# Performance work log

Hardware: AMD Instinct MI355X
Metric: run time of the kernel (lower is better)

Reference implementation:

```python
import jax, jax.numpy as jnp
import numpy as np

N, E, C, RB, H = 10000, 160000, 64, 8, 64
AVG_NEIGH = 16.0


def _sph(v):
    # component-normalized real spherical harmonics l=1,2,3 of unit vectors v [E,3]
    x, y, z = v[..., 0], v[..., 1], v[..., 2]
    s3, s5, s15 = 3.0 ** 0.5, 5.0 ** 0.5, 15.0 ** 0.5
    y1 = s3 * jnp.stack([x, y, z], -1)  # [E,3]
    y2 = jnp.stack([
        s15 * x * y,
        s15 * y * z,
        0.5 * s5 * (3.0 * z * z - 1.0),
        s15 * x * z,
        0.5 * s15 * (x * x - y * y),
    ], -1)  # [E,5]
    c1 = (35.0 / 8.0) ** 0.5
    c2 = 105.0 ** 0.5
    c3 = (21.0 / 8.0) ** 0.5
    c4 = (7.0 ** 0.5) / 2.0
    y3 = jnp.stack([
        c1 * y * (3.0 * x * x - y * y),
        c2 * x * y * z,
        c3 * y * (5.0 * z * z - 1.0),
        c4 * z * (5.0 * z * z - 3.0),
        c3 * x * (5.0 * z * z - 1.0),
        0.5 * c2 * z * (x * x - y * y),
        c1 * x * (x * x - y * y),
    ], -1)  # [E,7]
    return y1, y2, y3


def setup_inputs() -> dict:
    key = jax.random.key(0)
    ks = jax.random.split(key, 12)
    inp = {
        'vectors': jax.random.normal(ks[0], (E, 3), jnp.float32),
        'node_feats': jax.random.normal(ks[1], (N, C), jnp.float32),
        'radial_embedding': jax.random.normal(ks[2], (E, RB), jnp.float32),
        'W_up': jax.random.normal(ks[3], (C, C), jnp.float32) / np.sqrt(C),
        'mlp_w1': jax.random.normal(ks[4], (RB, H), jnp.float32) / np.sqrt(RB),
        'mlp_w2': jax.random.normal(ks[5], (H, H), jnp.float32) / np.sqrt(H),
        'mlp_w3': jax.random.normal(ks[6], (H, H), jnp.float32) / np.sqrt(H),
        'mlp_w4': jax.random.normal(ks[7], (H, 4 * C), jnp.float32) / np.sqrt(H),
        'W_down': jax.random.normal(ks[8], (4, C, C), jnp.float32) / np.sqrt(C),
        'senders': jax.random.randint(ks[9], (E,), 0, N, jnp.int32),
        'receivers': jax.random.randint(ks[10], (E,), 0, N, jnp.int32),
    }
    return inp


def reference(vectors, node_feats, radial_embedding, W_up, mlp_w1, mlp_w2, mlp_w3, mlp_w4, W_down, senders, receivers):
    n = node_feats.shape[0]
    # linear_up (scalars: plain channel mixing)
    x = node_feats @ W_up                                   # [N,C]
    sf = x[senders]                                         # [E,C] gather
    u = vectors / (jnp.linalg.norm(vectors, axis=-1, keepdims=True) + 1e-12)
    y1, y2, y3 = _sph(u)
    # radial MLP -> per-irrep mixing weights [E, 4C]
    h = jax.nn.silu(radial_embedding @ mlp_w1)
    h = jax.nn.silu(h @ mlp_w2)
    h = jax.nn.silu(h @ mlp_w3)
    mix = h @ mlp_w4
    m0, m1, m2, m3 = jnp.split(mix, 4, axis=-1)             # each [E,C]
    # tensor product of Cx0e with Y_l -> Cx(l), scaled by radial mix
    msg0 = sf * m0                                          # [E,C]
    msg1 = (sf * m1)[:, :, None] * y1[:, None, :]           # [E,C,3]
    msg2 = (sf * m2)[:, :, None] * y2[:, None, :]           # [E,C,5]
    msg3 = (sf * m3)[:, :, None] * y3[:, None, :]           # [E,C,7]
    inv = 1.0 / jnp.sqrt(jnp.asarray(AVG_NEIGH, msg0.dtype))
    seg = lambda m: jax.ops.segment_sum(m, receivers, num_segments=n) * inv
    o0, o1, o2, o3 = seg(msg0), seg(msg1), seg(msg2), seg(msg3)
    # linear_down: per-l channel mixing
    o0 = o0 @ W_down[0]
    o1 = jnp.einsum('ncm,cd->ndm', o1, W_down[1])
    o2 = jnp.einsum('ncm,cd->ndm', o2, W_down[2])
    o3 = jnp.einsum('ncm,cd->ndm', o3, W_down[3])
    return jnp.concatenate([o0, o1.reshape(n, -1), o2.reshape(n, -1), o3.reshape(n, -1)], axis=-1)  # [N, 16C]
```

## Files before the change

### kernel.cpp

```cpp
#include <hip/hip_runtime.h>
#include <math.h>

#define CC 64
typedef _Float16 f16;
typedef _Float16 half8_t __attribute__((ext_vector_type(8)));
typedef float f32x4 __attribute__((ext_vector_type(4)));

__device__ __forceinline__ float silu_f(float v) {
    return v / (1.0f + __expf(-v));
}

__global__ __launch_bounds__(256) void k_pre(
        const float* __restrict__ nf, const float* __restrict__ Wup,
        float* __restrict__ x, int N,
        const float* __restrict__ w1, const float* __restrict__ w2,
        const float* __restrict__ w3, const float* __restrict__ w4,
        const float* __restrict__ Wd,
        f16* __restrict__ wT1, f16* __restrict__ wT2,
        f16* __restrict__ wT3, f16* __restrict__ wT4,
        float* __restrict__ wpack,
        const int* __restrict__ rcv, int* __restrict__ cnt, int E) {
    int nb_up = (N * CC + 255) >> 8;
    int b = blockIdx.x;
    if (b < nb_up) {
        int tid = b * 256 + threadIdx.x;
        if (tid >= N * CC) return;
        int n = tid >> 6;
        int j = tid & 63;
        const float* nfr = nf + (size_t)n * CC;
        float acc = 0.f;
#pragma unroll
        for (int k = 0; k < CC; ++k) acc += nfr[k] * Wup[k * CC + j];
        x[tid] = acc;
    } else if (b < nb_up + 168) {
        int i = (b - nb_up) * 256 + threadIdx.x;
        if (i < 2048) {
            int n = i >> 5, k = i & 31;
            wT1[i] = (k < 8) ? (f16)w1[k * 64 + n] : (f16)0.f;
        } else if (i < 6144) {
            int j = i - 2048; int n = j >> 6, k = j & 63;
            wT2[j] = (f16)w2[k * 64 + n];
        } else if (i < 10240) {
            int j = i - 6144; int n = j >> 6, k = j & 63;
            wT3[j] = (f16)w3[k * 64 + n];
        } else if (i < 26624) {
            int j = i - 10240; int l = j >> 12; int r = j & 4095;
            int n = r >> 6, k = r & 63;
            wT4[j] = (f16)w4[k * 256 + l * 64 + n];
        } else if (i < 43008) {
            int j = i - 26624;
            int pos = j >> 2;
            int comp = j & 3;
            wpack[j] = 0.25f * Wd[comp * 4096 + pos];
        }
    } else {
        int e = (b - nb_up - 168) * 256 + threadIdx.x;
        if (e < E) atomicAdd(&cnt[rcv[e]], 1);
    }
}

__global__ __launch_bounds__(1024) void k_scan(const int* __restrict__ cnt,
        int* __restrict__ off, int* __restrict__ cur, int N) {
    __shared__ int wsum[16];
    int t = threadIdx.x;
    int wave = t >> 6, lane = t & 63;
    int per = (N + 1023) >> 10;
    int i0 = t * per;
    int s = 0;
    for (int j = 0; j < per; ++j) {
        int i = i0 + j;
        if (i < N) s += cnt[i];
    }
    int sc = s;
#pragma unroll
    for (int d = 1; d < 64; d <<= 1) {
        int u = __shfl_up(sc, d, 64);
        if (lane >= d) sc += u;
    }
    if (lane == 63) wsum[wave] = sc;
    __syncthreads();
    if (wave == 0) {
        int v = (lane < 16) ? wsum[lane] : 0;
        int s2 = v;
#pragma unroll
        for (int d = 1; d < 16; d <<= 1) {
            int u = __shfl_up(s2, d, 64);
            if (lane >= d) s2 += u;
        }
        if (lane < 16) wsum[lane] = s2;
    }
    __syncthreads();
    int base = ((wave > 0) ? wsum[wave - 1] : 0) + (sc - s);
    int run = base;
    for (int j = 0; j < per; ++j) {
        int i = i0 + j;
        if (i < N) { off[i] = run; cur[i] = run; run += cnt[i]; }
    }
    if (t == 1023) off[N] = run;
}

__global__ void k_fill(const int* __restrict__ rcv, const int* __restrict__ snd,
                       const float* __restrict__ vec, int* __restrict__ cur,
                       int* __restrict__ eid, int* __restrict__ sndp,
                       float* __restrict__ yb, int E) {
    int e = blockIdx.x * blockDim.x + threadIdx.x;
    if (e >= E) return;
    int p = atomicAdd(&cur[rcv[e]], 1);
    eid[p] = e;
    sndp[p] = snd[e];

    float vx = vec[(size_t)e * 3 + 0];
    float vy = vec[(size_t)e * 3 + 1];
    float vz = vec[(size_t)e * 3 + 2];
    float nrm = sqrtf(vx * vx + vy * vy + vz * vz) + 1e-12f;
    float rinv = 1.0f / nrm;
    float ux = vx * rinv, uy = vy * rinv, uz = vz * rinv;

    const float s3 = 1.7320508075688772f;
    const float s5 = 2.2360679774997896f;
    const float s15 = 3.8729833462074170f;
    const float c1 = 2.0916500663351889f;
    const float c2 = 10.246950765959598f;
    const float c3 = 1.6201851746019651f;
    const float c4 = 1.3228756555322954f;

    float zz = uz * uz, xx = ux * ux, yy = uy * uy;
    float4 r0 = {1.0f, s3 * ux, s3 * uy, s3 * uz};
    float4 r1 = {s15 * ux * uy, s15 * uy * uz, 0.5f * s5 * (3.f * zz - 1.f),
                 s15 * ux * uz};
    float4 r2 = {0.5f * s15 * (xx - yy), c1 * uy * (3.f * xx - yy),
                 c2 * ux * uy * uz, c3 * uy * (5.f * zz - 1.f)};
    float4 r3 = {c4 * uz * (5.f * zz - 3.f), c3 * ux * (5.f * zz - 1.f),
                 0.5f * c2 * uz * (xx - yy), c1 * ux * (xx - yy)};
    float* yr = yb + (size_t)p * 16;
    *(float4*)(yr + 0)  = r0;
    *(float4*)(yr + 4)  = r1;
    *(float4*)(yr + 8)  = r2;
    *(float4*)(yr + 12) = r3;
}

__global__ __launch_bounds__(128) void k_mlp(const float* __restrict__ rad,
        const f16* __restrict__ wT1, const f16* __restrict__ wT2,
        const f16* __restrict__ wT3, const f16* __restrict__ wT4,
        const int* __restrict__ eid, const int* __restrict__ sndp,
        const float* __restrict__ x, f16* __restrict__ mixp, int E) {
    __shared__ f16 act[64][72];

    int t = threadIdx.x;
    int e0 = blockIdx.x * 64;
    int lane = t & 63;
    int wid = t >> 6;
    int m0 = wid * 32;
    int fm = lane & 15;
    int q  = lane >> 4;

    const half8_t hz = {0, 0, 0, 0, 0, 0, 0, 0};

    float4 sfa[4], sfb[4];
#pragma unroll
    for (int it = 0; it < 4; ++it) {
        int row = (lane >> 3) + it * 8;
        int ci = e0 + m0 + row;
        int s = (ci < E) ? sndp[ci] : 0;
        const float* xr = x + (size_t)s * 64 + (lane & 7) * 8;
        sfa[it] = *(const float4*)xr;
        sfb[it] = *(const float4*)(xr + 4);
    }

    half8_t a0 = hz, a1 = hz;
    if (q == 0) {
        int ci0 = e0 + m0 + fm;
        if (ci0 < E) {
            int e = eid[ci0];
            float4 p0 = *(const float4*)(rad + (size_t)e * 8);
            float4 p1 = *(const float4*)(rad + (size_t)e * 8 + 4);
            a0 = (half8_t){(f16)p0.x, (f16)p0.y, (f16)p0.z, (f16)p0.w,
                           (f16)p1.x, (f16)p1.y, (f16)p1.z, (f16)p1.w};
        }
        int ci1 = e0 + m0 + 16 + fm;
        if (ci1 < E) {
            int e = eid[ci1];
            float4 p0 = *(const float4*)(rad + (size_t)e * 8);
            float4 p1 = *(const float4*)(rad + (size_t)e * 8 + 4);
            a1 = (half8_t){(f16)p0.x, (f16)p0.y, (f16)p0.z, (f16)p0.w,
                           (f16)p1.x, (f16)p1.y, (f16)p1.z, (f16)p1.w};
        }
    }
#pragma unroll
    for (int nt = 0; nt < 4; ++nt) {
        half8_t b = *(const half8_t*)(wT1 + ((nt * 16 + fm) << 5) + q * 8);
        f32x4 c0 = {0.f, 0.f, 0.f, 0.f};
        c0 = __builtin_amdgcn_mfma_f32_16x16x32_f16(a0, b, c0, 0, 0, 0);
        f32x4 c1 = {0.f, 0.f, 0.f, 0.f};
        c1 = __builtin_amdgcn_mfma_f32_16x16x32_f16(a1, b, c1, 0, 0, 0);
#pragma unroll
        for (int r = 0; r < 4; ++r) {
            act[m0 + q * 4 + r][nt * 16 + fm]      = (f16)silu_f(c0[r]);
            act[m0 + 16 + q * 4 + r][nt * 16 + fm] = (f16)silu_f(c1[r]);
        }
    }

    auto loadA = [&](int mbase, int kc) -> half8_t {
        return *(const half8_t*)&act[mbase + fm][kc + q * 8];
    };

    const f16* wts[2] = {wT2, wT3};
#pragma unroll
    for (int L = 0; L < 2; ++L) {
        const f16* wT = wts[L];
        half8_t a00 = loadA(m0, 0),      a01 = loadA(m0, 32);
        half8_t a10 = loadA(m0 + 16, 0), a11 = loadA(m0 + 16, 32);
#pragma unroll
        for (int nt = 0; nt < 4; ++nt) {
            const f16* wr = wT + ((nt * 16 + fm) << 6);
            half8_t b0 = *(const half8_t*)(wr + q * 8);
            half8_t b1 = *(const half8_t*)(wr + 32 + q * 8);
            f32x4 c0 = {0.f, 0.f, 0.f, 0.f};
            c0 = __builtin_amdgcn_mfma_f32_16x16x32_f16(a00, b0, c0, 0, 0, 0);
            c0 = __builtin_amdgcn_mfma_f32_16x16x32_f16(a01, b1, c0, 0, 0, 0);
            f32x4 c1 = {0.f, 0.f, 0.f, 0.f};
            c1 = __builtin_amdgcn_mfma_f32_16x16x32_f16(a10, b0, c1, 0, 0, 0);
            c1 = __builtin_amdgcn_mfma_f32_16x16x32_f16(a11, b1, c1, 0, 0, 0);
#pragma unroll
            for (int r = 0; r < 4; ++r) {
                act[m0 + q * 4 + r][nt * 16 + fm]      = (f16)silu_f(c0[r]);
                act[m0 + 16 + q * 4 + r][nt * 16 + fm] = (f16)silu_f(c1[r]);
            }
        }
    }

    half8_t A00 = loadA(m0, 0),      A01 = loadA(m0, 32);
    half8_t A10 = loadA(m0 + 16, 0), A11 = loadA(m0 + 16, 32);

#pragma unroll
    for (int l = 0; l < 4; ++l) {
        const f16* wT = wT4 + (l << 12);
#pragma unroll
        for (int nt = 0; nt < 4; ++nt) {
            const f16* wr = wT + ((nt * 16 + fm) << 6);
            half8_t b0 = *(const half8_t*)(wr + q * 8);
            half8_t b1 = *(const half8_t*)(wr + 32 + q * 8);
            f32x4 c0 = {0.f, 0.f, 0.f, 0.f};
            c0 = __builtin_amdgcn_mfma_f32_16x16x32_f16(A00, b0, c0, 0, 0, 0);
            c0 = __builtin_amdgcn_mfma_f32_16x16x32_f16(A01, b1, c0, 0, 0, 0);
            f32x4 c1 = {0.f, 0.f, 0.f, 0.f};
            c1 = __builtin_amdgcn_mfma_f32_16x16x32_f16(A10, b0, c1, 0, 0, 0);
            c1 = __builtin_amdgcn_mfma_f32_16x16x32_f16(A11, b1, c1, 0, 0, 0);
#pragma unroll
            for (int r = 0; r < 4; ++r) {
                act[m0 + q * 4 + r][nt * 16 + fm]      = (f16)c0[r];
                act[m0 + 16 + q * 4 + r][nt * 16 + fm] = (f16)c1[r];
            }
        }
#pragma unroll
        for (int it = 0; it < 4; ++it) {
            int row = (lane >> 3) + it * 8;
            int ci = e0 + m0 + row;
            if (ci < E) {
                half8_t v = *(const half8_t*)&act[m0 + row][(lane & 7) * 8];
                half8_t w;
                w[0] = (f16)((float)v[0] * sfa[it].x);
                w[1] = (f16)((float)v[1] * sfa[it].y);
                w[2] = (f16)((float)v[2] * sfa[it].z);
                w[3] = (f16)((float)v[3] * sfa[it].w);
                w[4] = (f16)((float)v[4] * sfb[it].x);
                w[5] = (f16)((float)v[5] * sfb[it].y);
                w[6] = (f16)((float)v[6] * sfb[it].z);
                w[7] = (f16)((float)v[7] * sfb[it].w);
                *(half8_t*)&mixp[(size_t)ci * 256 + l * 64 + (lane & 7) * 8] = w;
            }
        }
    }
}

__global__ __launch_bounds__(256) void k_gather(
        const f16* __restrict__ mixp, const float* __restrict__ yb,
        const int* __restrict__ off, const f32x4* __restrict__ wpack,
        float* __restrict__ out, int N) {
    __shared__ float sbuf[4][64 * 20];
    __shared__ float ybs[4][16][16];
    int wv = threadIdx.x >> 6;
    int lane = threadIdx.x & 63;
    int n = blockIdx.x * 4 + wv;
    if (n >= N) return;

    float o[16];
#pragma unroll
    for (int i = 0; i < 16; ++i) o[i] = 0.f;

    auto process = [&](int i, int j) {
        const float* yr = &ybs[wv][j][0];
        f32x4 A  = *(const f32x4*)(yr + 0);
        f32x4 B  = *(const f32x4*)(yr + 4);
        f32x4 Cv = *(const f32x4*)(yr + 8);
        f32x4 D  = *(const f32x4*)(yr + 12);
        const f16* mr = mixp + (size_t)i * 256;
        float t0 = (float)mr[lane];
        float t1 = (float)mr[64 + lane];
        float t2 = (float)mr[128 + lane];
        float t3 = (float)mr[192 + lane];
        o[0]  += t0;
        o[1]  += t1 * A.y;
        o[2]  += t1 * A.z;
        o[3]  += t1 * A.w;
        o[4]  += t2 * B.x;
        o[5]  += t2 * B.y;
        o[6]  += t2 * B.z;
        o[7]  += t2 * B.w;
        o[8]  += t2 * Cv.x;
        o[9]  += t3 * Cv.y;
        o[10] += t3 * Cv.z;
        o[11] += t3 * Cv.w;
        o[12] += t3 * D.x;
        o[13] += t3 * D.y;
        o[14] += t3 * D.z;
        o[15] += t3 * D.w;
    };

    int beg = off[n], end = off[n + 1];
    for (int cb = beg; cb < end; cb += 16) {
        int m = end - cb; if (m > 16) m = 16;
        if (lane < m * 4) {
            f32x4 v = *(const f32x4*)(yb + (size_t)cb * 16 + lane * 4);
            *(f32x4*)&ybs[wv][lane >> 2][(lane & 3) * 4] = v;
        }
        int j = 0;
        for (; j + 1 < m; j += 2) { process(cb + j, j); process(cb + j + 1, j + 1); }
        if (j < m) process(cb + j, j);
    }

    float* sw = sbuf[wv];
#pragma unroll
    for (int a = 0; a < 4; ++a) {
        f32x4 vq = {o[4 * a + 0], o[4 * a + 1], o[4 * a + 2], o[4 * a + 3]};
        *(f32x4*)&sw[lane * 20 + 4 * a] = vq;
    }

    f32x4 dA = {0.f, 0.f, 0.f, 0.f}, dB = dA, dC = dA, dD = dA;
#pragma unroll 2
    for (int c = 0; c < 64; ++c) {
        f32x4 q0 = *(const f32x4*)&sw[c * 20 + 0];
        f32x4 q1 = *(const f32x4*)&sw[c * 20 + 4];
        f32x4 q2 = *(const f32x4*)&sw[c * 20 + 8];
        f32x4 q3 = *(const f32x4*)&sw[c * 20 + 12];
        f32x4 wp = wpack[c * 64 + lane];
        f32x4 wA = {wp.x, wp.y, wp.y, wp.y};
        f32x4 wC4 = {wp.z, wp.w, wp.w, wp.w};
        dA += q0 * wA;
        dB += q1 * wp.z;
        dC += q2 * wC4;
        dD += q3 * wp.w;
    }

    float* outr = out + (size_t)n * 1024;
    outr[lane] = dA[0];
#pragma unroll
    for (int m = 0; m < 3; ++m) outr[64 + lane * 3 + m] = dA[1 + m];
    outr[256 + lane * 5 + 0] = dB[0];
    outr[256 + lane * 5 + 1] = dB[1];
    outr[256 + lane * 5 + 2] = dB[2];
    outr[256 + lane * 5 + 3] = dB[3];
    outr[256 + lane * 5 + 4] = dC[0];
    outr[576 + lane * 7 + 0] = dC[1];
    outr[576 + lane * 7 + 1] = dC[2];
    outr[576 + lane * 7 + 2] = dC[3];
    outr[576 + lane * 7 + 3] = dD[0];
    outr[576 + lane * 7 + 4] = dD[1];
    outr[576 + lane * 7 + 5] = dD[2];
    outr[576 + lane * 7 + 6] = dD[3];
}

extern "C" void kernel_launch(void* const* d_in, const int* in_sizes, int n_in,
                              void* d_out, int out_size, void* d_ws, size_t ws_size,
                              hipStream_t stream) {
    const float* vectors    = (const float*)d_in[0];
    const float* node_feats = (const float*)d_in[1];
    const float* radial     = (const float*)d_in[2];
    const float* W_up       = (const float*)d_in[3];
    const float* w1         = (const float*)d_in[4];
    const float* w2         = (const float*)d_in[5];
    const float* w3         = (const float*)d_in[6];
    const float* w4         = (const float*)d_in[7];
    const float* Wd         = (const float*)d_in[8];
    const int*   snd        = (const int*)d_in[9];
    const int*   rcv        = (const int*)d_in[10];
    float* out = (float*)d_out;

    int E = in_sizes[9];
    int N = in_sizes[1] / CC;

    f16*   wT1   = (f16*)d_ws;
    f16*   wT2   = wT1 + 2048;
    f16*   wT3   = wT2 + 4096;
    f16*   wT4   = wT3 + 4096;
    float* wpack = (float*)(wT4 + 16384);
    float* x     = wpack + 16384;
    float* yb    = x + (size_t)N * 64;
    f16*   mixp  = (f16*)(yb + (size_t)E * 16);
    int*   cnt   = (int*)(mixp + (size_t)E * 256);
    int*   off   = cnt + N;
    int*   cur   = off + (N + 1);
    int*   eid   = cur + N;
    int*   sndp  = eid + E;

    hipMemsetAsync(cnt, 0, (size_t)N * sizeof(int), stream);

    int nb_up = (N * CC + 255) / 256;
    int nb_hist = (E + 255) / 256;
    k_pre<<<nb_up + 168 + nb_hist, 256, 0, stream>>>(
        node_feats, W_up, x, N, w1, w2, w3, w4, Wd,
        wT1, wT2, wT3, wT4, wpack, rcv, cnt, E);
    k_scan<<<1, 1024, 0, stream>>>(cnt, off, cur, N);
    k_fill<<<(E + 255) / 256, 256, 0, stream>>>(rcv, snd, vectors, cur, eid, sndp, yb, E);
    k_mlp<<<(E + 63) / 64, 128, 0, stream>>>(radial, wT1, wT2, wT3, wT4,
                                             eid, sndp, x, mixp, E);
    k_gather<<<(N + 3) / 4, 256, 0, stream>>>(mixp, yb, off,
                                              (const f32x4*)wpack, out, N);
}
```

Measured before the change: 217.6 us.

## Split MLP output columns across warps and halve edges per block in k_mlp

k_mlp now handles 32 edges per block instead of 64. In the hidden layers the two warps split the output columns (two 16-column tiles each) rather than each owning its own 32 rows, with __syncthreads between layers. This doubles the block count and shrinks shared memory per block, aiming for more parallelism and occupancy. The cost is extra block-wide barriers, and each warp now loads the full A operand while reusing each weight fragment over fewer rows.

```diff
diff --git a/kernel.cpp b/kernel.cpp
--- a/kernel.cpp
+++ b/kernel.cpp
@@ -144,23 +144,24 @@
         const f16* __restrict__ wT3, const f16* __restrict__ wT4,
         const int* __restrict__ eid, const int* __restrict__ sndp,
         const float* __restrict__ x, f16* __restrict__ mixp, int E) {
-    __shared__ f16 act[64][72];
+    __shared__ f16 act[32][72];
 
     int t = threadIdx.x;
-    int e0 = blockIdx.x * 64;
+    int e0 = blockIdx.x * 32;
     int lane = t & 63;
     int wid = t >> 6;
-    int m0 = wid * 32;
     int fm = lane & 15;
     int q  = lane >> 4;
+    int nt0 = wid * 2;
+    int mb  = wid * 16;
 
     const half8_t hz = {0, 0, 0, 0, 0, 0, 0, 0};
 
-    float4 sfa[4], sfb[4];
-#pragma unroll
-    for (int it = 0; it < 4; ++it) {
+    float4 sfa[2], sfb[2];
+#pragma unroll
+    for (int it = 0; it < 2; ++it) {
         int row = (lane >> 3) + it * 8;
-        int ci = e0 + m0 + row;
+        int ci = e0 + mb + row;
         int s = (ci < E) ? sndp[ci] : 0;
         const float* xr = x + (size_t)s * 64 + (lane & 7) * 8;
         sfa[it] = *(const float4*)xr;
@@ -169,7 +170,7 @@
 
     half8_t a0 = hz, a1 = hz;
     if (q == 0) {
-        int ci0 = e0 + m0 + fm;
+        int ci0 = e0 + fm;
         if (ci0 < E) {
             int e = eid[ci0];
             float4 p0 = *(const float4*)(rad + (size_t)e * 8);
@@ -177,7 +178,7 @@
             a0 = (half8_t){(f16)p0.x, (f16)p0.y, (f16)p0.z, (f16)p0.w,
                            (f16)p1.x, (f16)p1.y, (f16)p1.z, (f16)p1.w};
         }
-        int ci1 = e0 + m0 + 16 + fm;
+        int ci1 = e0 + 16 + fm;
         if (ci1 < E) {
             int e = eid[ci1];
             float4 p0 = *(const float4*)(rad + (size_t)e * 8);
@@ -187,7 +188,8 @@
         }
     }
 #pragma unroll
-    for (int nt = 0; nt < 4; ++nt) {
+    for (int ntl = 0; ntl < 2; ++ntl) {
+        int nt = nt0 + ntl;
         half8_t b = *(const half8_t*)(wT1 + ((nt * 16 + fm) << 5) + q * 8);
         f32x4 c0 = {0.f, 0.f, 0.f, 0.f};
         c0 = __builtin_amdgcn_mfma_f32_16x16x32_f16(a0, b, c0, 0, 0, 0);
@@ -195,10 +197,11 @@
         c1 = __builtin_amdgcn_mfma_f32_16x16x32_f16(a1, b, c1, 0, 0, 0);
 #pragma unroll
         for (int r = 0; r < 4; ++r) {
-            act[m0 + q * 4 + r][nt * 16 + fm]      = (f16)silu_f(c0[r]);
-            act[m0 + 16 + q * 4 + r][nt * 16 + fm] = (f16)silu_f(c1[r]);
-        }
-    }
+            act[q * 4 + r][nt * 16 + fm]      = (f16)silu_f(c0[r]);
+            act[16 + q * 4 + r][nt * 16 + fm] = (f16)silu_f(c1[r]);
+        }
+    }
+    __syncthreads();
 
     auto loadA = [&](int mbase, int kc) -> half8_t {
         return *(const half8_t*)&act[mbase + fm][kc + q * 8];
@@ -208,10 +211,12 @@
 #pragma unroll
     for (int L = 0; L < 2; ++L) {
         const f16* wT = wts[L];
-        half8_t a00 = loadA(m0, 0),      a01 = loadA(m0, 32);
-        half8_t a10 = loadA(m0 + 16, 0), a11 = loadA(m0 + 16, 32);
-#pragma unroll
-        for (int nt = 0; nt < 4; ++nt) {
+        half8_t a00 = loadA(0, 0),  a01 = loadA(0, 32);
+        half8_t a10 = loadA(16, 0), a11 = loadA(16, 32);
+        __syncthreads();
+#pragma unroll
+        for (int ntl = 0; ntl < 2; ++ntl) {
+            int nt = nt0 + ntl;
             const f16* wr = wT + ((nt * 16 + fm) << 6);
             half8_t b0 = *(const half8_t*)(wr + q * 8);
             half8_t b1 = *(const half8_t*)(wr + 32 + q * 8);
@@ -223,14 +228,14 @@
             c1 = __builtin_amdgcn_mfma_f32_16x16x32_f16(a11, b1, c1, 0, 0, 0);
 #pragma unroll
             for (int r = 0; r < 4; ++r) {
-                act[m0 + q * 4 + r][nt * 16 + fm]      = (f16)silu_f(c0[r]);
-                act[m0 + 16 + q * 4 + r][nt * 16 + fm] = (f16)silu_f(c1[r]);
+                act[q * 4 + r][nt * 16 + fm]      = (f16)silu_f(c0[r]);
+                act[16 + q * 4 + r][nt * 16 + fm] = (f16)silu_f(c1[r]);
             }
         }
-    }
-
-    half8_t A00 = loadA(m0, 0),      A01 = loadA(m0, 32);
-    half8_t A10 = loadA(m0 + 16, 0), A11 = loadA(m0 + 16, 32);
+        __syncthreads();
+    }
+
+    half8_t A0 = loadA(mb, 0), A1 = loadA(mb, 32);
 
 #pragma unroll
     for (int l = 0; l < 4; ++l) {
@@ -241,23 +246,18 @@
             half8_t b0 = *(const half8_t*)(wr + q * 8);
             half8_t b1 = *(const half8_t*)(wr + 32 + q * 8);
             f32x4 c0 = {0.f, 0.f, 0.f, 0.f};
-            c0 = __builtin_amdgcn_mfma_f32_16x16x32_f16(A00, b0, c0, 0, 0, 0);
-            c0 = __builtin_amdgcn_mfma_f32_16x16x32_f16(A01, b1, c0, 0, 0, 0);
-            f32x4 c1 = {0.f, 0.f, 0.f, 0.f};
-            c1 = __builtin_amdgcn_mfma_f32_16x16x32_f16(A10, b0, c1, 0, 0, 0);
-            c1 = __builtin_amdgcn_mfma_f32_16x16x32_f16(A11, b1, c1, 0, 0, 0);
-#pragma unroll
-            for (int r = 0; r < 4; ++r) {
-                act[m0 + q * 4 + r][nt * 16 + fm]      = (f16)c0[r];
-                act[m0 + 16 + q * 4 + r][nt * 16 + fm] = (f16)c1[r];
-            }
-        }
-#pragma unroll
-        for (int it = 0; it < 4; ++it) {
+            c0 = __builtin_amdgcn_mfma_f32_16x16x32_f16(A0, b0, c0, 0, 0, 0);
+            c0 = __builtin_amdgcn_mfma_f32_16x16x32_f16(A1, b1, c0, 0, 0, 0);
+#pragma unroll
+            for (int r = 0; r < 4; ++r)
+                act[mb + q * 4 + r][nt * 16 + fm] = (f16)c0[r];
+        }
+#pragma unroll
+        for (int it = 0; it < 2; ++it) {
             int row = (lane >> 3) + it * 8;
-            int ci = e0 + m0 + row;
+            int ci = e0 + mb + row;
             if (ci < E) {
-                half8_t v = *(const half8_t*)&act[m0 + row][(lane & 7) * 8];
+                half8_t v = *(const half8_t*)&act[mb + row][(lane & 7) * 8];
                 half8_t w;
                 w[0] = (f16)((float)v[0] * sfa[it].x);
                 w[1] = (f16)((float)v[1] * sfa[it].y);
@@ -412,7 +412,7 @@
         wT1, wT2, wT3, wT4, wpack, rcv, cnt, E);
     k_scan<<<1, 1024, 0, stream>>>(cnt, off, cur, N);
     k_fill<<<(E + 255) / 256, 256, 0, stream>>>(rcv, snd, vectors, cur, eid, sndp, yb, E);
-    k_mlp<<<(E + 63) / 64, 128, 0, stream>>>(radial, wT1, wT2, wT3, wT4,
+    k_mlp<<<(E + 31) / 32, 128, 0, stream>>>(radial, wT1, wT2, wT3, wT4,
                                              eid, sndp, x, mixp, E);
     k_gather<<<(N + 3) / 4, 256, 0, stream>>>(mixp, yb, off,
                                               (const f32x4*)wpack, out, N);
```

Measured after the change: 233.7 us. 7.4% more time.
